# Performance work log

Hardware: AMD Instinct MI355X
Metric: run time of the kernel (lower is better)

Reference implementation:

```python
import jax, jax.numpy as jnp
import numpy as np

B, S, D, H = 2, 2048, 1024, 16
HD = D // H  # 64

def _make_freqs():
    # flux-style rotation matrices: [1,1,S,HD//2,2,2]
    theta = 10000.0
    inv = 1.0 / (theta ** (np.arange(0, HD, 2, dtype=np.float32) / HD))  # [HD//2]
    pos = np.arange(S, dtype=np.float32)
    ang = pos[:, None] * inv[None, :]  # [S, HD//2]
    cos, sin = np.cos(ang), np.sin(ang)
    rot = np.stack([np.stack([cos, -sin], -1), np.stack([sin, cos], -1)], -2)  # [S,HD//2,2,2]
    return jnp.asarray(rot[None, None], dtype=jnp.float32)

def setup_inputs() -> dict:
    key = jax.random.key(0)
    ks = jax.random.split(key, 9)
    sc = 1.0 / np.sqrt(D)
    return {
        "x": jax.random.normal(ks[0], (B, S, D), jnp.float32),
        "freqs": _make_freqs(),
        "Wq": jax.random.normal(ks[1], (D, D), jnp.float32) * sc,
        "bq": jax.random.normal(ks[2], (D,), jnp.float32) * 0.01,
        "Wk": jax.random.normal(ks[3], (D, D), jnp.float32) * sc,
        "bk": jax.random.normal(ks[4], (D,), jnp.float32) * 0.01,
        "Wv": jax.random.normal(ks[5], (D, D), jnp.float32) * sc,
        "bv": jax.random.normal(ks[6], (D,), jnp.float32) * 0.01,
        "Wo": jax.random.normal(ks[7], (D, D), jnp.float32) * sc,
        "bo": jax.random.normal(ks[8], (D,), jnp.float32) * 0.01,
    }

def _apply_rope(xq, xk, freqs):
    # xq/xk: [B,H,S,HD]; freqs: [1,1,S,HD//2,2,2]
    def rot(t):
        t_ = t.reshape(*t.shape[:-1], -1, 1, 2)  # [B,H,S,HD//2,1,2]
        out = freqs[..., 0] * t_[..., 0] + freqs[..., 1] * t_[..., 1]  # [B,H,S,HD//2,2]
        return out.reshape(t.shape).astype(t.dtype)
    return rot(xq), rot(xk)

def reference(x, freqs, Wq, bq, Wk, bk, Wv, bv, Wo, bo):
    b, s, _ = x.shape
    # QKV projections (torch Linear: x @ W.T + b)
    q = (x @ Wq.T + bq).reshape(b, s, H, HD).transpose(0, 2, 1, 3)  # [B,H,S,HD]
    k = (x @ Wk.T + bk).reshape(b, s, H, HD).transpose(0, 2, 1, 3)
    v = (x @ Wv.T + bv).reshape(b, s, H, HD).transpose(0, 2, 1, 3)
    q, k = _apply_rope(q, k, freqs)
    # scaled dot product attention, no mask, no dropout
    scale = 1.0 / jnp.sqrt(jnp.asarray(HD, x.dtype))
    scores = jnp.einsum("bhqd,bhkd->bhqk", q, k) * scale
    attn = jax.nn.softmax(scores, axis=-1)
    o = jnp.einsum("bhqk,bhkd->bhqd", attn, v)  # [B,H,S,HD]
    o = o.transpose(0, 2, 1, 3).reshape(b, s, D)
    return o @ Wo.T + bo
```

## Files before the change

kernel.cpp:

```cpp
#include <hip/hip_runtime.h>
#include <cmath>

#define B_ 2
#define S_ 2048
#define D_ 1024
#define H_ 16
#define HD_ 64
#define M_ 4096

typedef __attribute__((ext_vector_type(8))) short short8;
typedef __attribute__((ext_vector_type(4))) short short4v;
typedef __attribute__((ext_vector_type(4))) float f32x4;

__device__ __forceinline__ short f2bf(float x) {
    unsigned u = __builtin_bit_cast(unsigned, x);
    u += 0x7fffu + ((u >> 16) & 1u);
    return (short)(u >> 16);
}

__device__ __forceinline__ void gload_lds16(const short* g, short* l) {
    __builtin_amdgcn_global_load_lds(
        (const __attribute__((address_space(1))) unsigned int*)g,
        (__attribute__((address_space(3))) unsigned int*)l, 16, 0, 0);
}

__global__ __launch_bounds__(256) void cast_all_kernel(
    const float* __restrict__ x,  const float* __restrict__ Wq,
    const float* __restrict__ Wk, const float* __restrict__ Wv,
    const float* __restrict__ Wo,
    short* __restrict__ xb, short* __restrict__ Wqkvb, short* __restrict__ Wob)
{
    const size_t i = (size_t)blockIdx.x * 256 + threadIdx.x;
    const float* src; short* dst; size_t off;
    if (i < 1048576)      { src = x;  dst = xb;              off = i; }
    else if (i < 1310720) { src = Wq; dst = Wqkvb;           off = i - 1048576; }
    else if (i < 1572864) { src = Wk; dst = Wqkvb + 1048576; off = i - 1310720; }
    else if (i < 1835008) { src = Wv; dst = Wqkvb + 2097152; off = i - 1572864; }
    else                  { src = Wo; dst = Wob;             off = i - 1835008; }
    float4 v = ((const float4*)src)[off];
    short4v o = { f2bf(v.x), f2bf(v.y), f2bf(v.z), f2bf(v.w) };
    ((short4v*)dst)[off] = o;
}

template<int MODE, int TM, int TN>
__global__ __launch_bounds__(256) void gemm_chunk(
    const short* __restrict__ A, const short* __restrict__ Bw,
    const float* __restrict__ b0p, const float* __restrict__ b1p, const float* __restrict__ b2p,
    const float* __restrict__ freqs,
    void* __restrict__ out0, void* __restrict__ out1, void* __restrict__ out2)
{
    constexpr int RT = TM / 32, CT = TN / 32;
    __shared__ __align__(16) short As[4*TM*32];
    __shared__ __align__(16) short Bs[4*TN*32];
    const int t = threadIdx.x;
    const int w = t >> 6;
    const int lane = t & 63;
    const int qd = lane >> 4, l = lane & 15;
    const int n0 = blockIdx.x * TN, m0 = blockIdx.y * TM;
    const int wr = (w >> 1) * (TM/2), wc = (w & 1) * (TN/2);
    const int srow = lane >> 2;
    const int scol = (lane & 3) * 8;

    f32x4 acc[RT][CT] = {};

    for (int k0 = 0; k0 < 1024; k0 += 128) {
        __syncthreads();
        #pragma unroll
        for (int sub = 0; sub < 4; ++sub) {
            #pragma unroll
            for (int j = 0; j < TM/64; ++j) {
                const int rr = (j*4 + w) * 16;
                gload_lds16(A + (size_t)(m0 + rr + srow)*1024 + k0 + sub*32 + scol,
                            &As[sub*TM*32 + rr*32]);
            }
            #pragma unroll
            for (int j = 0; j < TN/64; ++j) {
                const int rr = (j*4 + w) * 16;
                gload_lds16(Bw + (size_t)(n0 + rr + srow)*1024 + k0 + sub*32 + scol,
                            &Bs[sub*TN*32 + rr*32]);
            }
        }
        __syncthreads();
        #pragma unroll
        for (int sub = 0; sub < 4; ++sub) {
            short8 af[RT], bf[CT];
            #pragma unroll
            for (int rt = 0; rt < RT; ++rt)
                af[rt] = *(const short8*)&As[sub*TM*32 + (wr + rt*16 + l)*32 + qd*8];
            #pragma unroll
            for (int ct = 0; ct < CT; ++ct)
                bf[ct] = *(const short8*)&Bs[sub*TN*32 + (wc + ct*16 + l)*32 + qd*8];
            #pragma unroll
            for (int rt = 0; rt < RT; ++rt)
                #pragma unroll
                for (int ct = 0; ct < CT; ++ct)
                    acc[rt][ct] = __builtin_amdgcn_mfma_f32_16x16x32_bf16(af[rt], bf[ct], acc[rt][ct], 0, 0, 0);
        }
    }

    if (MODE == 0) {
        float* out = (float*)out0;
        #pragma unroll
        for (int rt = 0; rt < RT; ++rt)
            #pragma unroll
            for (int ct = 0; ct < CT; ++ct) {
                const int n = n0 + wc + ct*16 + l;
                const float bias = b0p[n];
                #pragma unroll
                for (int r = 0; r < 4; ++r) {
                    const int m = m0 + wr + rt*16 + qd*4 + r;
                    out[(size_t)m*1024 + n] = acc[rt][ct][r] + bias;
                }
            }
    } else {
        const int sel = n0 >> 10;
        const int nb = n0 & 1023;
        const float* bias = (sel == 0) ? b0p : (sel == 1) ? b1p : b2p;
        if (sel < 2) {
            short* outg = (short*)((sel == 0) ? out0 : out1);
            #pragma unroll
            for (int rt = 0; rt < RT; ++rt)
                #pragma unroll
                for (int ct = 0; ct < CT; ++ct) {
                    const int d = nb + wc + ct*16 + l;
                    const float bsv = bias[d];
                    const int h = d >> 6, hd = d & 63;
                    #pragma unroll
                    for (int r = 0; r < 4; ++r) {
                        const int m = m0 + wr + rt*16 + qd*4 + r;
                        const int bb = m >> 11, s = m & 2047;
                        float val = acc[rt][ct][r] + bsv;
                        float pv = __shfl_xor(val, 1);
                        const float* f = freqs + (size_t)s*128 + (size_t)(hd >> 1)*4;
                        float o = (d & 1) ? (f[2]*pv + f[3]*val) : (f[0]*val + f[1]*pv);
                        outg[((size_t)(bb*16 + h)*2048 + s)*64 + hd] = f2bf(o);
                    }
                }
        } else {
            short* outv = (short*)out2;
            #pragma unroll
            for (int rt = 0; rt < RT; ++rt)
                #pragma unroll
                for (int ct = 0; ct < CT; ++ct) {
                    const int d = nb + wc + ct*16 + l;
                    const float bsv = bias[d];
                    const int h = d >> 6, hd = d & 63;
                    const int m0r = m0 + wr + rt*16 + qd*4;
                    const int bb = m0r >> 11, s0 = m0r & 2047;
                    short4v pk;
                    #pragma unroll
                    for (int r = 0; r < 4; ++r) pk[r] = f2bf(acc[rt][ct][r] + bsv);
                    *(short4v*)&outv[((size_t)(bb*16 + h)*64 + hd)*2048 + s0] = pk;
                }
        }
    }
}

__global__ __launch_bounds__(256) void attn_mfma(
    const short* __restrict__ qg, const short* __restrict__ kg,
    const short* __restrict__ vtg, short* __restrict__ og)
{
    __shared__ __align__(16) short KP[128*136];
    __shared__ __align__(16) short Vt[64*136];

    const int t = threadIdx.x;
    const int w = t >> 6;
    const int lane = t & 63;
    const int qd = lane >> 4, l = lane & 15;
    const int q0 = blockIdx.x * 128;
    const int bh = blockIdx.y;

    short8 qf[2][2];
    const short* qb = qg + ((size_t)bh*2048 + q0 + w*32)*64;
    #pragma unroll
    for (int rt = 0; rt < 2; ++rt)
        #pragma unroll
        for (int kf = 0; kf < 2; ++kf)
            qf[rt][kf] = *(const short8*)&qb[(rt*16 + l)*64 + kf*32 + qd*8];

    f32x4 oacc[2][4] = {};
    float lsum[2] = {};

    const short* kbase = kg  + (size_t)bh*2048*64;
    const short* vbase = vtg + (size_t)bh*64*2048;
    const float SC = 0.125f * 1.44269504088896340736f;

    for (int kt = 0; kt < 16; ++kt) {
        __syncthreads();
        {
            const short* src = kbase + (size_t)(kt*128 + (t>>1))*64 + (t&1)*32;
            short* dst = &KP[(t>>1)*136 + (t&1)*32];
            *(short8*)(dst+0)  = *(const short8*)(src+0);
            *(short8*)(dst+8)  = *(const short8*)(src+8);
            *(short8*)(dst+16) = *(const short8*)(src+16);
            *(short8*)(dst+24) = *(const short8*)(src+24);
        }
        {
            const short* src = vbase + (size_t)(t>>2)*2048 + kt*128 + (t&3)*32;
            short* dst = &Vt[(t>>2)*136 + (t&3)*32];
            *(short8*)(dst+0)  = *(const short8*)(src+0);
            *(short8*)(dst+8)  = *(const short8*)(src+8);
            *(short8*)(dst+16) = *(const short8*)(src+16);
            *(short8*)(dst+24) = *(const short8*)(src+24);
        }
        __syncthreads();

        f32x4 sacc[2][8] = {};
        #pragma unroll
        for (int ct = 0; ct < 8; ++ct) {
            short8 k0f = *(const short8*)&KP[(ct*16 + l)*136 + qd*8];
            short8 k1f = *(const short8*)&KP[(ct*16 + l)*136 + 32 + qd*8];
            #pragma unroll
            for (int rt = 0; rt < 2; ++rt) {
                sacc[rt][ct] = __builtin_amdgcn_mfma_f32_16x16x32_bf16(k0f, qf[rt][0], sacc[rt][ct], 0, 0, 0);
                sacc[rt][ct] = __builtin_amdgcn_mfma_f32_16x16x32_bf16(k1f, qf[rt][1], sacc[rt][ct], 0, 0, 0);
            }
        }
        __syncthreads();

        #pragma unroll
        for (int rt = 0; rt < 2; ++rt)
            #pragma unroll
            for (int ct = 0; ct < 8; ++ct) {
                short4v pk;
                #pragma unroll
                for (int r = 0; r < 4; ++r) {
                    float p = exp2f(sacc[rt][ct][r] * SC);
                    lsum[rt] += p;
                    pk[r] = f2bf(p);
                }
                *(short4v*)&KP[(w*32 + rt*16 + l)*136 + ct*16 + qd*4] = pk;
            }

        #pragma unroll
        for (int kf = 0; kf < 4; ++kf) {
            short8 pa0 = *(const short8*)&KP[(w*32 +  0 + l)*136 + kf*32 + qd*8];
            short8 pa1 = *(const short8*)&KP[(w*32 + 16 + l)*136 + kf*32 + qd*8];
            #pragma unroll
            for (int ht = 0; ht < 4; ++ht) {
                short8 vb = *(const short8*)&Vt[(ht*16 + l)*136 + kf*32 + qd*8];
                oacc[0][ht] = __builtin_amdgcn_mfma_f32_16x16x32_bf16(pa0, vb, oacc[0][ht], 0, 0, 0);
                oacc[1][ht] = __builtin_amdgcn_mfma_f32_16x16x32_bf16(pa1, vb, oacc[1][ht], 0, 0, 0);
            }
        }
    }

    #pragma unroll
    for (int rt = 0; rt < 2; ++rt) {
        lsum[rt] += __shfl_xor(lsum[rt], 16);
        lsum[rt] += __shfl_xor(lsum[rt], 32);
    }
    float inv[2][4];
    #pragma unroll
    for (int rt = 0; rt < 2; ++rt)
        #pragma unroll
        for (int r = 0; r < 4; ++r)
            inv[rt][r] = 1.0f / __shfl(lsum[rt], qd*4 + r);

    const int bb = bh >> 4, h = bh & 15;
    #pragma unroll
    for (int rt = 0; rt < 2; ++rt)
        #pragma unroll
        for (int ht = 0; ht < 4; ++ht)
            #pragma unroll
            for (int r = 0; r < 4; ++r) {
                const int s = q0 + w*32 + rt*16 + qd*4 + r;
                og[((size_t)bb*2048 + s)*1024 + h*64 + ht*16 + l] =
                    f2bf(oacc[rt][ht][r] * inv[rt][r]);
            }
}

extern "C" void kernel_launch(void* const* d_in, const int* in_sizes, int n_in,
                              void* d_out, int out_size, void* d_ws, size_t ws_size,
                              hipStream_t stream)
{
    const float* x  = (const float*)d_in[0];
    const float* fr = (const float*)d_in[1];
    const float* Wq = (const float*)d_in[2];
    const float* bq = (const float*)d_in[3];
    const float* Wk = (const float*)d_in[4];
    const float* bk = (const float*)d_in[5];
    const float* Wv = (const float*)d_in[6];
    const float* bv = (const float*)d_in[7];
    const float* Wo = (const float*)d_in[8];
    const float* bo = (const float*)d_in[9];
    float* out = (float*)d_out;

    short* ws    = (short*)d_ws;
    short* xb    = ws;
    short* Wqkvb = xb    + 4194304;
    short* Wob   = Wqkvb + 3145728;
    short* qg    = Wob   + 1048576;
    short* kg    = qg    + 4194304;
    short* vtg   = kg    + 4194304;
    short* og    = vtg   + 4194304;

    cast_all_kernel<<<8192, 256, 0, stream>>>(x, Wq, Wk, Wv, Wo, xb, Wqkvb, Wob);
    gemm_chunk<1,128,64><<<dim3(48, 32), 256, 0, stream>>>(xb, Wqkvb, bq, bk, bv, fr, qg, kg, vtg);
    attn_mfma<<<dim3(16, 32), 256, 0, stream>>>(qg, kg, vtg, og);
    gemm_chunk<0,64,64><<<dim3(16, 64), 256, 0, stream>>>(og, Wob, bo, nullptr, nullptr, nullptr,
                                                          out, nullptr, nullptr);
}
```

Baseline: 248.7 us.

## Fold softmax scale into Q, compute row sums via MFMA, retune GEMM tiles

```diff
diff --git a/kernel.cpp b/kernel.cpp
--- a/kernel.cpp
+++ b/kernel.cpp
@@ -1,4 +1,5 @@
 #include <hip/hip_runtime.h>
+#include <hip/hip_bf16.h>
 #include <cmath>
 
 #define B_ 2
@@ -16,6 +17,10 @@
     unsigned u = __builtin_bit_cast(unsigned, x);
     u += 0x7fffu + ((u >> 16) & 1u);
     return (short)(u >> 16);
+}
+__device__ __forceinline__ unsigned pk2(float a, float b) {
+    __hip_bfloat162 h = __float22bfloat162_rn(make_float2(a, b));
+    unsigned u; __builtin_memcpy(&u, &h, 4); return u;
 }
 
 __device__ __forceinline__ void gload_lds16(const short* g, short* l) {
@@ -38,11 +43,10 @@
     else if (i < 1835008) { src = Wv; dst = Wqkvb + 2097152; off = i - 1572864; }
     else                  { src = Wo; dst = Wob;             off = i - 1835008; }
     float4 v = ((const float4*)src)[off];
-    short4v o = { f2bf(v.x), f2bf(v.y), f2bf(v.z), f2bf(v.w) };
-    ((short4v*)dst)[off] = o;
-}
-
-template<int MODE, int TM, int TN>
+    ((int2*)dst)[off] = make_int2((int)pk2(v.x, v.y), (int)pk2(v.z, v.w));
+}
+
+template<int MODE, int TM, int TN, int SUBS>
 __global__ __launch_bounds__(256) void gemm_chunk(
     const short* __restrict__ A, const short* __restrict__ Bw,
     const float* __restrict__ b0p, const float* __restrict__ b1p, const float* __restrict__ b2p,
@@ -50,8 +54,8 @@
     void* __restrict__ out0, void* __restrict__ out1, void* __restrict__ out2)
 {
     constexpr int RT = TM / 32, CT = TN / 32;
-    __shared__ __align__(16) short As[4*TM*32];
-    __shared__ __align__(16) short Bs[4*TN*32];
+    __shared__ __align__(16) short As[SUBS*TM*32];
+    __shared__ __align__(16) short Bs[SUBS*TN*32];
     const int t = threadIdx.x;
     const int w = t >> 6;
     const int lane = t & 63;
@@ -63,10 +67,10 @@
 
     f32x4 acc[RT][CT] = {};
 
-    for (int k0 = 0; k0 < 1024; k0 += 128) {
-        __syncthreads();
-        #pragma unroll
-        for (int sub = 0; sub < 4; ++sub) {
+    for (int k0 = 0; k0 < 1024; k0 += 32*SUBS) {
+        __syncthreads();
+        #pragma unroll
+        for (int sub = 0; sub < SUBS; ++sub) {
             #pragma unroll
             for (int j = 0; j < TM/64; ++j) {
                 const int rr = (j*4 + w) * 16;
@@ -82,7 +86,7 @@
         }
         __syncthreads();
         #pragma unroll
-        for (int sub = 0; sub < 4; ++sub) {
+        for (int sub = 0; sub < SUBS; ++sub) {
             short8 af[RT], bf[CT];
             #pragma unroll
             for (int rt = 0; rt < RT; ++rt)
@@ -118,6 +122,7 @@
         const float* bias = (sel == 0) ? b0p : (sel == 1) ? b1p : b2p;
         if (sel < 2) {
             short* outg = (short*)((sel == 0) ? out0 : out1);
+            const float scl = (sel == 0) ? 0.125f * 1.44269504088896340736f : 1.0f;
             #pragma unroll
             for (int rt = 0; rt < RT; ++rt)
                 #pragma unroll
@@ -133,7 +138,7 @@
                         float pv = __shfl_xor(val, 1);
                         const float* f = freqs + (size_t)s*128 + (size_t)(hd >> 1)*4;
                         float o = (d & 1) ? (f[2]*pv + f[3]*val) : (f[0]*val + f[1]*pv);
-                        outg[((size_t)(bb*16 + h)*2048 + s)*64 + hd] = f2bf(o);
+                        outg[((size_t)(bb*16 + h)*2048 + s)*64 + hd] = f2bf(o * scl);
                     }
                 }
         } else {
@@ -147,10 +152,10 @@
                     const int h = d >> 6, hd = d & 63;
                     const int m0r = m0 + wr + rt*16 + qd*4;
                     const int bb = m0r >> 11, s0 = m0r & 2047;
-                    short4v pk;
-                    #pragma unroll
-                    for (int r = 0; r < 4; ++r) pk[r] = f2bf(acc[rt][ct][r] + bsv);
-                    *(short4v*)&outv[((size_t)(bb*16 + h)*64 + hd)*2048 + s0] = pk;
+                    int2 pkv = make_int2(
+                        (int)pk2(acc[rt][ct][0] + bsv, acc[rt][ct][1] + bsv),
+                        (int)pk2(acc[rt][ct][2] + bsv, acc[rt][ct][3] + bsv));
+                    *(int2*)&outv[((size_t)(bb*16 + h)*64 + hd)*2048 + s0] = pkv;
                 }
         }
     }
@@ -178,12 +183,14 @@
         for (int kf = 0; kf < 2; ++kf)
             qf[rt][kf] = *(const short8*)&qb[(rt*16 + l)*64 + kf*32 + qd*8];
 
+    const short one_bf = (short)0x3F80;
+    const short8 ones = { one_bf, one_bf, one_bf, one_bf, one_bf, one_bf, one_bf, one_bf };
+
     f32x4 oacc[2][4] = {};
-    float lsum[2] = {};
+    f32x4 sumacc[2] = {};
 
     const short* kbase = kg  + (size_t)bh*2048*64;
     const short* vbase = vtg + (size_t)bh*64*2048;
-    const float SC = 0.125f * 1.44269504088896340736f;
 
     for (int kt = 0; kt < 16; ++kt) {
         __syncthreads();
@@ -222,20 +229,20 @@
         for (int rt = 0; rt < 2; ++rt)
             #pragma unroll
             for (int ct = 0; ct < 8; ++ct) {
-                short4v pk;
-                #pragma unroll
-                for (int r = 0; r < 4; ++r) {
-                    float p = exp2f(sacc[rt][ct][r] * SC);
-                    lsum[rt] += p;
-                    pk[r] = f2bf(p);
-                }
-                *(short4v*)&KP[(w*32 + rt*16 + l)*136 + ct*16 + qd*4] = pk;
+                float p0 = __builtin_amdgcn_exp2f(sacc[rt][ct][0]);
+                float p1 = __builtin_amdgcn_exp2f(sacc[rt][ct][1]);
+                float p2 = __builtin_amdgcn_exp2f(sacc[rt][ct][2]);
+                float p3 = __builtin_amdgcn_exp2f(sacc[rt][ct][3]);
+                *(int2*)&KP[(w*32 + rt*16 + l)*136 + ct*16 + qd*4] =
+                    make_int2((int)pk2(p0, p1), (int)pk2(p2, p3));
             }
 
         #pragma unroll
         for (int kf = 0; kf < 4; ++kf) {
             short8 pa0 = *(const short8*)&KP[(w*32 +  0 + l)*136 + kf*32 + qd*8];
             short8 pa1 = *(const short8*)&KP[(w*32 + 16 + l)*136 + kf*32 + qd*8];
+            sumacc[0] = __builtin_amdgcn_mfma_f32_16x16x32_bf16(pa0, ones, sumacc[0], 0, 0, 0);
+            sumacc[1] = __builtin_amdgcn_mfma_f32_16x16x32_bf16(pa1, ones, sumacc[1], 0, 0, 0);
             #pragma unroll
             for (int ht = 0; ht < 4; ++ht) {
                 short8 vb = *(const short8*)&Vt[(ht*16 + l)*136 + kf*32 + qd*8];
@@ -245,17 +252,12 @@
         }
     }
 
-    #pragma unroll
-    for (int rt = 0; rt < 2; ++rt) {
-        lsum[rt] += __shfl_xor(lsum[rt], 16);
-        lsum[rt] += __shfl_xor(lsum[rt], 32);
-    }
     float inv[2][4];
     #pragma unroll
     for (int rt = 0; rt < 2; ++rt)
         #pragma unroll
         for (int r = 0; r < 4; ++r)
-            inv[rt][r] = 1.0f / __shfl(lsum[rt], qd*4 + r);
+            inv[rt][r] = 1.0f / sumacc[rt][r];
 
     const int bb = bh >> 4, h = bh & 15;
     #pragma unroll
@@ -296,8 +298,8 @@
     short* og    = vtg   + 4194304;
 
     cast_all_kernel<<<8192, 256, 0, stream>>>(x, Wq, Wk, Wv, Wo, xb, Wqkvb, Wob);
-    gemm_chunk<1,128,64><<<dim3(48, 32), 256, 0, stream>>>(xb, Wqkvb, bq, bk, bv, fr, qg, kg, vtg);
+    gemm_chunk<1,128,128,2><<<dim3(24, 32), 256, 0, stream>>>(xb, Wqkvb, bq, bk, bv, fr, qg, kg, vtg);
     attn_mfma<<<dim3(16, 32), 256, 0, stream>>>(qg, kg, vtg, og);
-    gemm_chunk<0,64,64><<<dim3(16, 64), 256, 0, stream>>>(og, Wob, bo, nullptr, nullptr, nullptr,
-                                                          out, nullptr, nullptr);
-}
+    gemm_chunk<0,128,64,2><<<dim3(16, 32), 256, 0, stream>>>(og, Wob, bo, nullptr, nullptr, nullptr,
+                                                             out, nullptr, nullptr);
+}
```

After: 253.0 us. No clear change (+1.7%).
